# Performance work log

Measured on AMD Instinct MI355X. Metric: run time of the kernel, lower is better.

Reference implementation:

```python
import jax, jax.numpy as jnp
import numpy as np

N = 50000        # nodes
E = 800000       # edges (avg degree 16)
G = 64           # graphs in batch
F_IN = 9
OUT = 10


def setup_inputs() -> dict:
    key = jax.random.key(0)
    ks = jax.random.split(key, 20)
    def w(k, fi, fo):
        return jax.random.normal(k, (fi, fo), dtype=jnp.float32) * (1.0 / np.sqrt(fi))
    inp = {
        "x": jax.random.normal(ks[0], (N, F_IN), dtype=jnp.float32),
        "edge_index": jax.random.randint(ks[1], (2, E), 0, N, dtype=jnp.int64),
        "batch": jnp.sort(jax.random.randint(ks[2], (N,), 0, G, dtype=jnp.int64)),
        # GCNConv weights (PyG: x @ W then normalized scatter-add, + bias)
        "W1": w(ks[3], F_IN, 128), "b1": jnp.zeros((128,), jnp.float32),
        "W2": w(ks[4], 128, 256),  "b2": jnp.zeros((256,), jnp.float32),
        "W3": w(ks[5], 256, 256),  "b3": jnp.zeros((256,), jnp.float32),
        "W4": w(ks[6], 256, 256),  "b4": jnp.zeros((256,), jnp.float32),
        # dense head
        "Wl2": w(ks[7], 256, 128), "bl2": jnp.zeros((128,), jnp.float32),
        "Wl3": w(ks[8], 128, 128), "bl3": jnp.zeros((128,), jnp.float32),
        "Wl":  w(ks[9], 128, OUT), "bl":  jnp.zeros((OUT,), jnp.float32),
    }
    return inp


def reference(x, edge_index, batch, W1, b1, W2, b2, W3, b3, W4, b4,
              Wl2, bl2, Wl3, bl3, Wl, bl):
    # GCNConv with self-loops and symmetric deg^{-1/2} normalization
    loops = jnp.arange(N, dtype=edge_index.dtype)
    src = jnp.concatenate([edge_index[0], loops])   # [E+N]
    dst = jnp.concatenate([edge_index[1], loops])
    deg = jax.ops.segment_sum(jnp.ones_like(src, dtype=x.dtype), dst, num_segments=N)
    dinv = jax.lax.rsqrt(deg)                        # deg >= 1 due to self-loops
    norm = (dinv[src] * dinv[dst])[:, None]          # [E+N, 1]

    def conv(h, W, b):
        msg = (h @ W)[src] * norm                    # gather + normalize
        return jax.ops.segment_sum(msg, dst, num_segments=N) + b

    h = jax.nn.relu(conv(x, W1, b1))
    h = jax.nn.relu(conv(h, W2, b2))
    h = jax.nn.relu(conv(h, W3, b3))
    h = conv(h, W4, b4)                              # no relu before pool
    g = jax.ops.segment_max(h, batch, num_segments=G)  # global_max_pool -> [G, 256]
    g = jax.nn.relu(g @ Wl2 + bl2)
    g = jax.nn.relu(g @ Wl3 + bl3)
    out = g @ Wl + bl                                # [G, OUT]
    return jnp.squeeze(out)
```

## Files before the change

kernel.cpp:

```cpp
#include <hip/hip_runtime.h>
#include <float.h>

#define NN 50000
#define NE 800000
#define NG 64
#define CAP 64

typedef __attribute__((ext_vector_type(8))) _Float16 f16x8;
typedef __attribute__((ext_vector_type(4))) float f32x4;
typedef __attribute__((ext_vector_type(4))) _Float16 half4;
typedef __attribute__((ext_vector_type(2))) _Float16 half2v;
typedef unsigned int u32;

__device__ __forceinline__ unsigned f2mono(float f) {
  unsigned b = __float_as_uint(f);
  return (b & 0x80000000u) ? ~b : (b | 0x80000000u);
}
__device__ __forceinline__ float mono2f(unsigned u) {
  unsigned b = (u & 0x80000000u) ? (u & 0x7fffffffu) : ~u;
  return __uint_as_float(b);
}
__device__ __forceinline__ void gl_lds16(const void* g, void* l) {
  __builtin_amdgcn_global_load_lds((const __attribute__((address_space(1))) u32*)g,
                                   (__attribute__((address_space(3))) u32*)l, 16, 0, 0);
}

__global__ void k_count(const int* __restrict__ src, const int* __restrict__ dst,
                        int* __restrict__ cnt, int* __restrict__ col) {
  int e = blockIdx.x * blockDim.x + threadIdx.x;
  if (e >= NE) return;
  int d = dst[e];
  int s = src[e];
  if ((unsigned)d >= NN || (unsigned)s >= NN) return;
  int pos = atomicAdd(&cnt[d], 1);
  if (pos < CAP) col[d * CAP + pos] = s;
}

__global__ void k_dinv(const int* __restrict__ cnt, float* __restrict__ dinv,
                       const float* __restrict__ x, float* __restrict__ xs) {
  int v = blockIdx.x * blockDim.x + threadIdx.x;
  if (v >= NN) return;
  float d = rsqrtf((float)cnt[v] + 1.0f);
  dinv[v] = d;
#pragma unroll
  for (int i = 0; i < 9; ++i) xs[v * 9 + i] = x[v * 9 + i] * d;
}

__global__ void k_splitw(const float* __restrict__ W, _Float16* __restrict__ Wh,
                         _Float16* __restrict__ Wl, int K, int Nc) {
  int i = blockIdx.x * blockDim.x + threadIdx.x;
  if (i >= K * Nc) return;
  int k = i / Nc, n = i - k * Nc;
  float w = W[i];
  _Float16 h = (_Float16)w;
  _Float16 l = (_Float16)(w - (float)h);
  Wh[(size_t)n * K + k] = h;
  Wl[(size_t)n * K + k] = l;
}

__global__ __launch_bounds__(256) void k_agg9(const float* __restrict__ xs,
                                              float* __restrict__ out,
                                              const int* __restrict__ cnt,
                                              const int* __restrict__ col,
                                              const float* __restrict__ dinv) {
  int v = (blockIdx.x * 256 + threadIdx.x) >> 4;
  int l = threadIdx.x & 15;
  if (v >= NN) return;
  int c = cnt[v]; if (c > CAP) c = CAP;
  const int* cl = col + v * CAP;
  float acc = (l < 9) ? xs[v * 9 + l] : 0.0f;
  int j = 0;
  for (; j + 4 <= c; j += 4) {
    int4 u = *(const int4*)(cl + j);
    float a0 = (l < 9) ? xs[u.x * 9 + l] : 0.f;
    float a1 = (l < 9) ? xs[u.y * 9 + l] : 0.f;
    float a2 = (l < 9) ? xs[u.z * 9 + l] : 0.f;
    float a3 = (l < 9) ? xs[u.w * 9 + l] : 0.f;
    acc += (a0 + a1) + (a2 + a3);
  }
  for (; j < c; ++j) {
    int u = cl[j];
    if (l < 9) acc += xs[u * 9 + l];
  }
  if (l < 9) out[v * 9 + l] = acc * dinv[v];
}

__global__ __launch_bounds__(256) void k_gemm9(const float* __restrict__ in,
                                               const float* __restrict__ W,
                                               const float* __restrict__ bias,
                                               const float* __restrict__ dinv,
                                               _Float16* __restrict__ out) {
  __shared__ float sW[9 * 128];
  __shared__ float sb[128];
  int t = threadIdx.x;
  if (t < 128) sb[t] = bias[t];
  for (int i = t; i < 9 * 128; i += 256) sW[i] = W[i];
  __syncthreads();
  int r = blockIdx.x * 2 + (t >> 7);
  int c = t & 127;
  if (r >= NN) return;
  float acc = sb[c];
#pragma unroll
  for (int i = 0; i < 9; ++i) acc += in[r * 9 + i] * sW[i * 128 + c];
  out[r * 128 + c] = (_Float16)(fmaxf(acc, 0.0f) * dinv[r]);
}

__global__ __launch_bounds__(256) void k_agg128(const half2v* __restrict__ h,
                                                half2v* __restrict__ out,
                                                const int* __restrict__ cnt,
                                                const int* __restrict__ col,
                                                const float* __restrict__ dinv) {
  int w = (blockIdx.x * 256 + threadIdx.x) >> 6;
  int lane = threadIdx.x & 63;
  if (w >= NN) return;
  half2v s = h[(size_t)w * 64 + lane];
  float ax = (float)s.x, ay = (float)s.y;
  int c = cnt[w]; if (c > CAP) c = CAP;
  const int* cl = col + w * CAP;
  int j = 0;
  for (; j + 4 <= c; j += 4) {
    int4 u = *(const int4*)(cl + j);
    half2v t0 = h[(size_t)u.x * 64 + lane];
    half2v t1 = h[(size_t)u.y * 64 + lane];
    half2v t2 = h[(size_t)u.z * 64 + lane];
    half2v t3 = h[(size_t)u.w * 64 + lane];
    ax += ((float)t0.x + (float)t1.x) + ((float)t2.x + (float)t3.x);
    ay += ((float)t0.y + (float)t1.y) + ((float)t2.y + (float)t3.y);
  }
  for (; j < c; ++j) {
    int u = cl[j];
    half2v tv = h[(size_t)u * 64 + lane];
    ax += (float)tv.x; ay += (float)tv.y;
  }
  float di = dinv[w];
  half2v o;
  o.x = (_Float16)(ax * di);
  o.y = (_Float16)(ay * di);
  out[(size_t)w * 64 + lane] = o;
}

__global__ __launch_bounds__(256) void k_agg256(const half4* __restrict__ h,
                                                half4* __restrict__ out,
                                                const int* __restrict__ cnt,
                                                const int* __restrict__ col,
                                                const float* __restrict__ dinv) {
  int w = (blockIdx.x * 256 + threadIdx.x) >> 6;
  int lane = threadIdx.x & 63;
  if (w >= NN) return;
  half4 s = h[(size_t)w * 64 + lane];
  float ax = (float)s.x, ay = (float)s.y, az = (float)s.z, aw = (float)s.w;
  int c = cnt[w]; if (c > CAP) c = CAP;
  const int* cl = col + w * CAP;
  int j = 0;
  for (; j + 4 <= c; j += 4) {
    int4 u = *(const int4*)(cl + j);
    half4 t0 = h[(size_t)u.x * 64 + lane];
    half4 t1 = h[(size_t)u.y * 64 + lane];
    half4 t2 = h[(size_t)u.z * 64 + lane];
    half4 t3 = h[(size_t)u.w * 64 + lane];
    ax += ((float)t0.x + (float)t1.x) + ((float)t2.x + (float)t3.x);
    ay += ((float)t0.y + (float)t1.y) + ((float)t2.y + (float)t3.y);
    az += ((float)t0.z + (float)t1.z) + ((float)t2.z + (float)t3.z);
    aw += ((float)t0.w + (float)t1.w) + ((float)t2.w + (float)t3.w);
  }
  for (; j < c; ++j) {
    int u = cl[j];
    half4 tv = h[(size_t)u * 64 + lane];
    ax += (float)tv.x; ay += (float)tv.y; az += (float)tv.z; aw += (float)tv.w;
  }
  float di = dinv[w];
  half4 o;
  o.x = (_Float16)(ax * di);
  o.y = (_Float16)(ay * di);
  o.z = (_Float16)(az * di);
  o.w = (_Float16)(aw * di);
  out[(size_t)w * 64 + lane] = o;
}

__global__ __launch_bounds__(256) void k_mm(const _Float16* __restrict__ A,
                                            const _Float16* __restrict__ Bh,
                                            const _Float16* __restrict__ Bl,
                                            const float* __restrict__ bias,
                                            _Float16* __restrict__ C,
                                            const float* __restrict__ dinv,
                                            const int* __restrict__ batch,
                                            unsigned* __restrict__ gpool,
                                            int M, int K, int Nc, int mode) {
  __shared__ __align__(16) _Float16 Alds[128 * 64];
  __shared__ __align__(16) _Float16 Bhl[128 * 64];
  __shared__ __align__(16) _Float16 Bll[128 * 64];
  int t = threadIdx.x;
  int wave = t >> 6, lane = t & 63;
  int wm = wave & 1, wn = wave >> 1;
  int rowBase = blockIdx.x * 128;
  int colBase = blockIdx.y * 128;
  int lm = lane & 15;
  int q  = lane >> 4;

  int srl = wave * 32 + (lane >> 3);
  int sj  = lane & 7;
  int ssw = lane >> 3;
  int gseg = sj ^ ssw;

  f32x4 acc[4][4];
#pragma unroll
  for (int i = 0; i < 4; ++i)
#pragma unroll
    for (int j = 0; j < 4; ++j) acc[i][j] = (f32x4){0.f, 0.f, 0.f, 0.f};

  int nit = K >> 6;
  for (int it = 0; it < nit; ++it) {
    __syncthreads();
#pragma unroll
    for (int c = 0; c < 4; ++c) {
      int rl = srl + c * 8;
      int ga = rowBase + rl; if (ga > M - 1) ga = M - 1;
      int gb = colBase + rl;
      unsigned off = (unsigned)it * 64 + gseg * 8;
      int ldst = (wave * 32 + c * 8) * 64 + lane * 8;
      gl_lds16(A  + (size_t)ga * K + off, Alds + ldst);
      gl_lds16(Bh + (size_t)gb * K + off, Bhl + ldst);
      gl_lds16(Bl + (size_t)gb * K + off, Bll + ldst);
    }
    __syncthreads();

#pragma unroll
    for (int s2 = 0; s2 < 2; ++s2) {
      int slotq = ((s2 << 2) | q);
      f16x8 vbh[4], vbl[4];
#pragma unroll
      for (int ni = 0; ni < 4; ++ni) {
        int rB = wn * 64 + ni * 16 + lm;
        int slot = slotq ^ (lm & 7);
        vbh[ni] = *(const f16x8*)(Bhl + rB * 64 + slot * 8);
        vbl[ni] = *(const f16x8*)(Bll + rB * 64 + slot * 8);
      }
#pragma unroll
      for (int mi = 0; mi < 4; ++mi) {
        int rA = wm * 64 + mi * 16 + lm;
        int slot = slotq ^ (lm & 7);
        f16x8 va = *(const f16x8*)(Alds + rA * 64 + slot * 8);
#pragma unroll
        for (int ni = 0; ni < 4; ++ni) {
          acc[mi][ni] = __builtin_amdgcn_mfma_f32_16x16x32_f16(va, vbh[ni], acc[mi][ni], 0, 0, 0);
          acc[mi][ni] = __builtin_amdgcn_mfma_f32_16x16x32_f16(va, vbl[ni], acc[mi][ni], 0, 0, 0);
        }
      }
    }
  }

  int rowOff = (lane >> 4) * 4;
  if (mode == 2) {
    __syncthreads();
    unsigned* ldsPool = (unsigned*)Alds;
    for (int i = t; i < 4 * 256; i += 256) ldsPool[i] = 0u;
    __syncthreads();
    int b0 = batch[rowBase];
#pragma unroll
    for (int mi = 0; mi < 4; ++mi) {
#pragma unroll
      for (int ni = 0; ni < 4; ++ni) {
        int gc = colBase + wn * 64 + ni * 16 + lm;
        float bsv = bias[gc];
#pragma unroll
        for (int r = 0; r < 4; ++r) {
          int gr = rowBase + wm * 64 + mi * 16 + rowOff + r;
          if (gr < M) {
            float v = acc[mi][ni][r] + bsv;
            int idx = batch[gr] - b0;
            if (idx < 0) idx = 0;
            if (idx > 3) idx = 3;
            atomicMax(&ldsPool[idx * 256 + gc], f2mono(v));
          }
        }
      }
    }
    __syncthreads();
#pragma unroll
    for (int s4 = 0; s4 < 4; ++s4) {
      unsigned mv = ldsPool[s4 * 256 + t];
      int gb = b0 + s4;
      if (mv && gb < NG) atomicMax(&gpool[gb * 256 + t], mv);
    }
  } else {
#pragma unroll
    for (int mi = 0; mi < 4; ++mi) {
#pragma unroll
      for (int ni = 0; ni < 4; ++ni) {
        int gc = colBase + wn * 64 + ni * 16 + lm;
        float bsv = bias[gc];
#pragma unroll
        for (int r = 0; r < 4; ++r) {
          int gr = rowBase + wm * 64 + mi * 16 + rowOff + r;
          if (gr < M) {
            float v = fmaxf(acc[mi][ni][r] + bsv, 0.0f);
            C[(size_t)gr * Nc + gc] = (_Float16)(v * dinv[gr]);
          }
        }
      }
    }
  }
}

__global__ __launch_bounds__(256) void k_head(const unsigned* __restrict__ g,
                                              const float* __restrict__ Wl2, const float* __restrict__ bl2,
                                              const float* __restrict__ Wl3, const float* __restrict__ bl3,
                                              const float* __restrict__ Wl, const float* __restrict__ bl,
                                              float* __restrict__ out) {
  __shared__ float s0[256];
  __shared__ float s1[128];
  __shared__ float s2[128];
  int b = blockIdx.x, t = threadIdx.x;
  s0[t] = mono2f(g[b * 256 + t]);
  __syncthreads();
  if (t < 128) {
    float acc = bl2[t];
    for (int k = 0; k < 256; ++k) acc += s0[k] * Wl2[k * 128 + t];
    s1[t] = fmaxf(acc, 0.0f);
  }
  __syncthreads();
  if (t < 128) {
    float acc = bl3[t];
    for (int k = 0; k < 128; ++k) acc += s1[k] * Wl3[k * 128 + t];
    s2[t] = fmaxf(acc, 0.0f);
  }
  __syncthreads();
  if (t < 10) {
    float acc = bl[t];
    for (int k = 0; k < 128; ++k) acc += s2[k] * Wl[k * 10 + t];
    out[b * 10 + t] = acc;
  }
}

extern "C" void kernel_launch(void* const* d_in, const int* in_sizes, int n_in,
                              void* d_out, int out_size, void* d_ws, size_t ws_size,
                              hipStream_t stream) {
  const float* x   = (const float*)d_in[0];
  const int* eidx  = (const int*)d_in[1];
  const int* batch = (const int*)d_in[2];
  const float* W1 = (const float*)d_in[3];   const float* b1 = (const float*)d_in[4];
  const float* W2 = (const float*)d_in[5];   const float* b2 = (const float*)d_in[6];
  const float* W3 = (const float*)d_in[7];   const float* b3 = (const float*)d_in[8];
  const float* W4 = (const float*)d_in[9];   const float* b4 = (const float*)d_in[10];
  const float* Wl2 = (const float*)d_in[11]; const float* bl2 = (const float*)d_in[12];
  const float* Wl3 = (const float*)d_in[13]; const float* bl3 = (const float*)d_in[14];
  const float* Wl  = (const float*)d_in[15]; const float* bl  = (const float*)d_in[16];
  float* out = (float*)d_out;

  _Float16* bufA = (_Float16*)d_ws;
  _Float16* bufB = bufA + (size_t)NN * 256;
  int* cnt  = (int*)(bufB + (size_t)NN * 256);
  float* dinv = (float*)(cnt + NN);
  int* col  = (int*)(dinv + NN);
  unsigned* g = (unsigned*)(col + (size_t)NN * CAP);
  _Float16* W2h = (_Float16*)(g + NG * 256);
  _Float16* W2l = W2h + 256 * 128;
  _Float16* W3h = W2l + 256 * 128;
  _Float16* W3l = W3h + 256 * 256;
  _Float16* W4h = W3l + 256 * 256;
  _Float16* W4l = W4h + 256 * 256;
  float* xs = (float*)bufA;
  float* agg9out = (float*)bufB;

  const int* src = eidx;
  const int* dst = eidx + NE;

  hipMemsetAsync(cnt, 0, NN * sizeof(int), stream);
  hipMemsetAsync(g, 0, NG * 256 * sizeof(unsigned), stream);

  k_count<<<(NE + 255) / 256, 256, 0, stream>>>(src, dst, cnt, col);
  k_dinv<<<(NN + 255) / 256, 256, 0, stream>>>(cnt, dinv, x, xs);

  k_splitw<<<(128 * 256 + 255) / 256, 256, 0, stream>>>(W2, W2h, W2l, 128, 256);
  k_splitw<<<(256 * 256 + 255) / 256, 256, 0, stream>>>(W3, W3h, W3l, 256, 256);
  k_splitw<<<(256 * 256 + 255) / 256, 256, 0, stream>>>(W4, W4h, W4l, 256, 256);

  k_agg9<<<(NN + 15) / 16, 256, 0, stream>>>(xs, agg9out, cnt, col, dinv);
  k_gemm9<<<NN / 2, 256, 0, stream>>>(agg9out, W1, b1, dinv, bufA);

  dim3 gmm((NN + 127) / 128, 2);

  k_agg128<<<(NN + 3) / 4, 256, 0, stream>>>((const half2v*)bufA, (half2v*)bufB, cnt, col, dinv);
  k_mm<<<gmm, 256, 0, stream>>>(bufB, W2h, W2l, b2, bufA, dinv, batch, g, NN, 128, 256, 1);

  k_agg256<<<(NN + 3) / 4, 256, 0, stream>>>((const half4*)bufA, (half4*)bufB, cnt, col, dinv);
  k_mm<<<gmm, 256, 0, stream>>>(bufB, W3h, W3l, b3, bufA, dinv, batch, g, NN, 256, 256, 1);

  k_agg256<<<(NN + 3) / 4, 256, 0, stream>>>((const half4*)bufA, (half4*)bufB, cnt, col, dinv);
  k_mm<<<gmm, 256, 0, stream>>>(bufB, W4h, W4l, b4, bufA, dinv, batch, g, NN, 256, 256, 2);

  k_head<<<NG, 256, 0, stream>>>(g, Wl2, bl2, Wl3, bl3, Wl, bl, out);
}
```

Measured before the change: 455.0 us.

## Process four nodes per wave in aggregation with 16-bit neighbor indices

The aggregation kernels now handle four destination nodes per wave and interleave their neighbor gathers in a common loop up to the smallest degree. This is meant to keep more independent loads in flight per wave. The neighbor list is stored as 16-bit indices, which is valid because the node count is below 65536, halving index traffic. Separately, the three weight-split launches are merged into one, and the pool-buffer memset is folded into the dinv kernel, saving launches. The cost is 4x fewer waves and more registers per wave, which may lower occupancy.

```diff
diff --git a/kernel.cpp b/kernel.cpp
--- a/kernel.cpp
+++ b/kernel.cpp
@@ -11,6 +11,7 @@
 typedef __attribute__((ext_vector_type(4))) _Float16 half4;
 typedef __attribute__((ext_vector_type(2))) _Float16 half2v;
 typedef unsigned int u32;
+typedef unsigned short u16;
 
 __device__ __forceinline__ unsigned f2mono(float f) {
   unsigned b = __float_as_uint(f);
@@ -26,30 +27,30 @@
 }
 
 __global__ void k_count(const int* __restrict__ src, const int* __restrict__ dst,
-                        int* __restrict__ cnt, int* __restrict__ col) {
-  int e = blockIdx.x * blockDim.x + threadIdx.x;
+                        int* __restrict__ cnt, u16* __restrict__ col) {
+  int e = blockIdx.x * 256 + threadIdx.x;
   if (e >= NE) return;
   int d = dst[e];
   int s = src[e];
   if ((unsigned)d >= NN || (unsigned)s >= NN) return;
   int pos = atomicAdd(&cnt[d], 1);
-  if (pos < CAP) col[d * CAP + pos] = s;
+  if (pos < CAP) col[d * CAP + pos] = (u16)s;
 }
 
 __global__ void k_dinv(const int* __restrict__ cnt, float* __restrict__ dinv,
-                       const float* __restrict__ x, float* __restrict__ xs) {
+                       const float* __restrict__ x, float* __restrict__ xs,
+                       unsigned* __restrict__ g) {
   int v = blockIdx.x * blockDim.x + threadIdx.x;
   if (v >= NN) return;
+  if (v < NG * 256) g[v] = 0u;
   float d = rsqrtf((float)cnt[v] + 1.0f);
   dinv[v] = d;
 #pragma unroll
   for (int i = 0; i < 9; ++i) xs[v * 9 + i] = x[v * 9 + i] * d;
 }
 
-__global__ void k_splitw(const float* __restrict__ W, _Float16* __restrict__ Wh,
-                         _Float16* __restrict__ Wl, int K, int Nc) {
-  int i = blockIdx.x * blockDim.x + threadIdx.x;
-  if (i >= K * Nc) return;
+__device__ __forceinline__ void splitw1(const float* W, _Float16* Wh, _Float16* Wl,
+                                        int i, int K, int Nc) {
   int k = i / Nc, n = i - k * Nc;
   float w = W[i];
   _Float16 h = (_Float16)w;
@@ -57,25 +58,36 @@
   Wh[(size_t)n * K + k] = h;
   Wl[(size_t)n * K + k] = l;
 }
+__global__ void k_splitw3(const float* __restrict__ W2, const float* __restrict__ W3,
+                          const float* __restrict__ W4,
+                          _Float16* __restrict__ W2h, _Float16* __restrict__ W2l,
+                          _Float16* __restrict__ W3h, _Float16* __restrict__ W3l,
+                          _Float16* __restrict__ W4h, _Float16* __restrict__ W4l) {
+  int i = blockIdx.x * 256 + threadIdx.x;
+  const int n2 = 128 * 256, n3 = 256 * 256;
+  if (i < n2) splitw1(W2, W2h, W2l, i, 128, 256);
+  else if (i < n2 + n3) splitw1(W3, W3h, W3l, i - n2, 256, 256);
+  else if (i < n2 + 2 * n3) splitw1(W4, W4h, W4l, i - n2 - n3, 256, 256);
+}
 
 __global__ __launch_bounds__(256) void k_agg9(const float* __restrict__ xs,
                                               float* __restrict__ out,
                                               const int* __restrict__ cnt,
-                                              const int* __restrict__ col,
+                                              const u16* __restrict__ col,
                                               const float* __restrict__ dinv) {
   int v = (blockIdx.x * 256 + threadIdx.x) >> 4;
   int l = threadIdx.x & 15;
   if (v >= NN) return;
   int c = cnt[v]; if (c > CAP) c = CAP;
-  const int* cl = col + v * CAP;
+  const u16* cl = col + (size_t)v * CAP;
   float acc = (l < 9) ? xs[v * 9 + l] : 0.0f;
   int j = 0;
   for (; j + 4 <= c; j += 4) {
-    int4 u = *(const int4*)(cl + j);
-    float a0 = (l < 9) ? xs[u.x * 9 + l] : 0.f;
-    float a1 = (l < 9) ? xs[u.y * 9 + l] : 0.f;
-    float a2 = (l < 9) ? xs[u.z * 9 + l] : 0.f;
-    float a3 = (l < 9) ? xs[u.w * 9 + l] : 0.f;
+    ushort4 u = *(const ushort4*)(cl + j);
+    float a0 = (l < 9) ? xs[(int)u.x * 9 + l] : 0.f;
+    float a1 = (l < 9) ? xs[(int)u.y * 9 + l] : 0.f;
+    float a2 = (l < 9) ? xs[(int)u.z * 9 + l] : 0.f;
+    float a3 = (l < 9) ? xs[(int)u.w * 9 + l] : 0.f;
     acc += (a0 + a1) + (a2 + a3);
   }
   for (; j < c; ++j) {
@@ -105,76 +117,108 @@
   out[r * 128 + c] = (_Float16)(fmaxf(acc, 0.0f) * dinv[r]);
 }
 
+#define G4_128(CL, J, AX, AY) {                          \
+    ushort4 u = *(const ushort4*)((CL) + (J));           \
+    half2v t0 = h[(size_t)u.x * 64 + lane];              \
+    half2v t1 = h[(size_t)u.y * 64 + lane];              \
+    half2v t2 = h[(size_t)u.z * 64 + lane];              \
+    half2v t3 = h[(size_t)u.w * 64 + lane];              \
+    AX += ((float)t0.x + (float)t1.x) + ((float)t2.x + (float)t3.x); \
+    AY += ((float)t0.y + (float)t1.y) + ((float)t2.y + (float)t3.y); }
 __global__ __launch_bounds__(256) void k_agg128(const half2v* __restrict__ h,
                                                 half2v* __restrict__ out,
                                                 const int* __restrict__ cnt,
-                                                const int* __restrict__ col,
+                                                const u16* __restrict__ col,
                                                 const float* __restrict__ dinv) {
-  int w = (blockIdx.x * 256 + threadIdx.x) >> 6;
+  int gw = (blockIdx.x * 256 + threadIdx.x) >> 6;
   int lane = threadIdx.x & 63;
-  if (w >= NN) return;
-  half2v s = h[(size_t)w * 64 + lane];
-  float ax = (float)s.x, ay = (float)s.y;
-  int c = cnt[w]; if (c > CAP) c = CAP;
-  const int* cl = col + w * CAP;
+  int w0 = gw * 4;
+  if (w0 >= NN) return;
+  float ax[4], ay[4];
+  int c[4];
+  const u16* cl[4];
+#pragma unroll
+  for (int nd = 0; nd < 4; ++nd) {
+    int wv = w0 + nd;
+    half2v s = h[(size_t)wv * 64 + lane];
+    ax[nd] = (float)s.x; ay[nd] = (float)s.y;
+    int cc = cnt[wv]; if (cc > CAP) cc = CAP;
+    c[nd] = cc;
+    cl[nd] = col + (size_t)wv * CAP;
+  }
+  int mc = min(min(c[0], c[1]), min(c[2], c[3]));
   int j = 0;
-  for (; j + 4 <= c; j += 4) {
-    int4 u = *(const int4*)(cl + j);
-    half2v t0 = h[(size_t)u.x * 64 + lane];
-    half2v t1 = h[(size_t)u.y * 64 + lane];
-    half2v t2 = h[(size_t)u.z * 64 + lane];
-    half2v t3 = h[(size_t)u.w * 64 + lane];
-    ax += ((float)t0.x + (float)t1.x) + ((float)t2.x + (float)t3.x);
-    ay += ((float)t0.y + (float)t1.y) + ((float)t2.y + (float)t3.y);
-  }
-  for (; j < c; ++j) {
-    int u = cl[j];
-    half2v tv = h[(size_t)u * 64 + lane];
-    ax += (float)tv.x; ay += (float)tv.y;
-  }
-  float di = dinv[w];
-  half2v o;
-  o.x = (_Float16)(ax * di);
-  o.y = (_Float16)(ay * di);
-  out[(size_t)w * 64 + lane] = o;
-}
-
+  for (; j + 4 <= mc; j += 4) {
+#pragma unroll
+    for (int nd = 0; nd < 4; ++nd) G4_128(cl[nd], j, ax[nd], ay[nd]);
+  }
+#pragma unroll
+  for (int nd = 0; nd < 4; ++nd) {
+    int jj = j;
+    for (; jj + 4 <= c[nd]; jj += 4) G4_128(cl[nd], jj, ax[nd], ay[nd]);
+    for (; jj < c[nd]; ++jj) {
+      half2v tv = h[(size_t)cl[nd][jj] * 64 + lane];
+      ax[nd] += (float)tv.x; ay[nd] += (float)tv.y;
+    }
+    float d = dinv[w0 + nd];
+    half2v o;
+    o.x = (_Float16)(ax[nd] * d); o.y = (_Float16)(ay[nd] * d);
+    out[(size_t)(w0 + nd) * 64 + lane] = o;
+  }
+}
+
+#define G4_256(CL, J, AX, AY, AZ, AW) {                  \
+    ushort4 u = *(const ushort4*)((CL) + (J));           \
+    half4 t0 = h[(size_t)u.x * 64 + lane];               \
+    half4 t1 = h[(size_t)u.y * 64 + lane];               \
+    half4 t2 = h[(size_t)u.z * 64 + lane];               \
+    half4 t3 = h[(size_t)u.w * 64 + lane];               \
+    AX += ((float)t0.x + (float)t1.x) + ((float)t2.x + (float)t3.x); \
+    AY += ((float)t0.y + (float)t1.y) + ((float)t2.y + (float)t3.y); \
+    AZ += ((float)t0.z + (float)t1.z) + ((float)t2.z + (float)t3.z); \
+    AW += ((float)t0.w + (float)t1.w) + ((float)t2.w + (float)t3.w); }
 __global__ __launch_bounds__(256) void k_agg256(const half4* __restrict__ h,
                                                 half4* __restrict__ out,
                                                 const int* __restrict__ cnt,
-                                                const int* __restrict__ col,
+                                                const u16* __restrict__ col,
                                                 const float* __restrict__ dinv) {
-  int w = (blockIdx.x * 256 + threadIdx.x) >> 6;
+  int gw = (blockIdx.x * 256 + threadIdx.x) >> 6;
   int lane = threadIdx.x & 63;
-  if (w >= NN) return;
-  half4 s = h[(size_t)w * 64 + lane];
-  float ax = (float)s.x, ay = (float)s.y, az = (float)s.z, aw = (float)s.w;
-  int c = cnt[w]; if (c > CAP) c = CAP;
-  const int* cl = col + w * CAP;
+  int w0 = gw * 4;
+  if (w0 >= NN) return;
+  float ax[4], ay[4], az[4], aw[4];
+  int c[4];
+  const u16* cl[4];
+#pragma unroll
+  for (int nd = 0; nd < 4; ++nd) {
+    int wv = w0 + nd;
+    half4 s = h[(size_t)wv * 64 + lane];
+    ax[nd] = (float)s.x; ay[nd] = (float)s.y; az[nd] = (float)s.z; aw[nd] = (float)s.w;
+    int cc = cnt[wv]; if (cc > CAP) cc = CAP;
+    c[nd] = cc;
+    cl[nd] = col + (size_t)wv * CAP;
+  }
+  int mc = min(min(c[0], c[1]), min(c[2], c[3]));
   int j = 0;
-  for (; j + 4 <= c; j += 4) {
-    int4 u = *(const int4*)(cl + j);
-    half4 t0 = h[(size_t)u.x * 64 + lane];
-    half4 t1 = h[(size_t)u.y * 64 + lane];
-    half4 t2 = h[(size_t)u.z * 64 + lane];
-    half4 t3 = h[(size_t)u.w * 64 + lane];
-    ax += ((float)t0.x + (float)t1.x) + ((float)t2.x + (float)t3.x);
-    ay += ((float)t0.y + (float)t1.y) + ((float)t2.y + (float)t3.y);
-    az += ((float)t0.z + (float)t1.z) + ((float)t2.z + (float)t3.z);
-    aw += ((float)t0.w + (float)t1.w) + ((float)t2.w + (float)t3.w);
-  }
-  for (; j < c; ++j) {
-    int u = cl[j];
-    half4 tv = h[(size_t)u * 64 + lane];
-    ax += (float)tv.x; ay += (float)tv.y; az += (float)tv.z; aw += (float)tv.w;
-  }
-  float di = dinv[w];
-  half4 o;
-  o.x = (_Float16)(ax * di);
-  o.y = (_Float16)(ay * di);
-  o.z = (_Float16)(az * di);
-  o.w = (_Float16)(aw * di);
-  out[(size_t)w * 64 + lane] = o;
+  for (; j + 4 <= mc; j += 4) {
+#pragma unroll
+    for (int nd = 0; nd < 4; ++nd) G4_256(cl[nd], j, ax[nd], ay[nd], az[nd], aw[nd]);
+  }
+#pragma unroll
+  for (int nd = 0; nd < 4; ++nd) {
+    int jj = j;
+    for (; jj + 4 <= c[nd]; jj += 4) G4_256(cl[nd], jj, ax[nd], ay[nd], az[nd], aw[nd]);
+    for (; jj < c[nd]; ++jj) {
+      half4 tv = h[(size_t)cl[nd][jj] * 64 + lane];
+      ax[nd] += (float)tv.x; ay[nd] += (float)tv.y;
+      az[nd] += (float)tv.z; aw[nd] += (float)tv.w;
+    }
+    float d = dinv[w0 + nd];
+    half4 o;
+    o.x = (_Float16)(ax[nd] * d); o.y = (_Float16)(ay[nd] * d);
+    o.z = (_Float16)(az[nd] * d); o.w = (_Float16)(aw[nd] * d);
+    out[(size_t)(w0 + nd) * 64 + lane] = o;
+  }
 }
 
 __global__ __launch_bounds__(256) void k_mm(const _Float16* __restrict__ A,
@@ -351,7 +395,7 @@
   _Float16* bufB = bufA + (size_t)NN * 256;
   int* cnt  = (int*)(bufB + (size_t)NN * 256);
   float* dinv = (float*)(cnt + NN);
-  int* col  = (int*)(dinv + NN);
+  u16* col  = (u16*)(dinv + NN);
   unsigned* g = (unsigned*)(col + (size_t)NN * CAP);
   _Float16* W2h = (_Float16*)(g + NG * 256);
   _Float16* W2l = W2h + 256 * 128;
@@ -366,27 +410,26 @@
   const int* dst = eidx + NE;
 
   hipMemsetAsync(cnt, 0, NN * sizeof(int), stream);
-  hipMemsetAsync(g, 0, NG * 256 * sizeof(unsigned), stream);
 
   k_count<<<(NE + 255) / 256, 256, 0, stream>>>(src, dst, cnt, col);
-  k_dinv<<<(NN + 255) / 256, 256, 0, stream>>>(cnt, dinv, x, xs);
-
-  k_splitw<<<(128 * 256 + 255) / 256, 256, 0, stream>>>(W2, W2h, W2l, 128, 256);
-  k_splitw<<<(256 * 256 + 255) / 256, 256, 0, stream>>>(W3, W3h, W3l, 256, 256);
-  k_splitw<<<(256 * 256 + 255) / 256, 256, 0, stream>>>(W4, W4h, W4l, 256, 256);
+  k_dinv<<<(NN + 255) / 256, 256, 0, stream>>>(cnt, dinv, x, xs, g);
+
+  k_splitw3<<<(128 * 256 + 2 * 256 * 256 + 255) / 256, 256, 0, stream>>>(
+      W2, W3, W4, W2h, W2l, W3h, W3l, W4h, W4l);
 
   k_agg9<<<(NN + 15) / 16, 256, 0, stream>>>(xs, agg9out, cnt, col, dinv);
   k_gemm9<<<NN / 2, 256, 0, stream>>>(agg9out, W1, b1, dinv, bufA);
 
   dim3 gmm((NN + 127) / 128, 2);
-
-  k_agg128<<<(NN + 3) / 4, 256, 0, stream>>>((const half2v*)bufA, (half2v*)bufB, cnt, col, dinv);
+  int aggGrid = ((NN + 3) / 4 * 64 + 255) / 256;
+
+  k_agg128<<<aggGrid, 256, 0, stream>>>((const half2v*)bufA, (half2v*)bufB, cnt, col, dinv);
   k_mm<<<gmm, 256, 0, stream>>>(bufB, W2h, W2l, b2, bufA, dinv, batch, g, NN, 128, 256, 1);
 
-  k_agg256<<<(NN + 3) / 4, 256, 0, stream>>>((const half4*)bufA, (half4*)bufB, cnt, col, dinv);
+  k_agg256<<<aggGrid, 256, 0, stream>>>((const half4*)bufA, (half4*)bufB, cnt, col, dinv);
   k_mm<<<gmm, 256, 0, stream>>>(bufB, W3h, W3l, b3, bufA, dinv, batch, g, NN, 256, 256, 1);
 
-  k_agg256<<<(NN + 3) / 4, 256, 0, stream>>>((const half4*)bufA, (half4*)bufB, cnt, col, dinv);
+  k_agg256<<<aggGrid, 256, 0, stream>>>((const half4*)bufA, (half4*)bufB, cnt, col, dinv);
   k_mm<<<gmm, 256, 0, stream>>>(bufB, W4h, W4l, b4, bufA, dinv, batch, g, NN, 256, 256, 2);
 
   k_head<<<NG, 256, 0, stream>>>(g, Wl2, bl2, Wl3, bl3, Wl, bl, out);
```

New measurement: 467.2 us. 2.7% more time.
